# Kernel tuning notes

Measured on AMD Instinct MI355X. Metric: run time of the kernel, lower is better.

The kernel has to match this reference:

```python
import jax, jax.numpy as jnp
import numpy as np

D = 256  # subgraph_width
N_CLASSES = 10
EPS = 1e-5  # torch LayerNorm default


def _layernorm(x, g, b):
    mu = jnp.mean(x, axis=-1, keepdims=True)
    var = jnp.var(x, axis=-1, keepdims=True)
    return (x - mu) * jax.lax.rsqrt(var + EPS) * g + b


def setup_inputs() -> dict:
    key = jax.random.key(0)
    ks = jax.random.split(key, 16)
    B, T, N = 64, 512, 512
    traj = jax.random.normal(ks[0], (B, T, 2), dtype=jnp.float32)
    labels = jax.random.randint(ks[1], (B,), 0, N_CLASSES)
    h = jax.random.normal(ks[2], (B, N, D), dtype=jnp.float32)
    valid_len = jnp.maximum(jax.random.randint(ks[3], (B,), 0, N), 1)
    s = 0.02
    params = dict(
        emb=jax.random.normal(ks[4], (N_CLASSES, D), dtype=jnp.float32) * s,
        w_mlp=jax.random.normal(ks[5], (2, D), dtype=jnp.float32) * s,
        b_mlp=jnp.zeros((D,), jnp.float32),
        ln_g=jnp.ones((D,), jnp.float32),
        ln_b=jnp.zeros((D,), jnp.float32),
        wq=jax.random.normal(ks[6], (D, D), dtype=jnp.float32) * s,
        bq=jnp.zeros((D,), jnp.float32),
        wk=jax.random.normal(ks[7], (D, D), dtype=jnp.float32) * s,
        bk=jnp.zeros((D,), jnp.float32),
        wv=jax.random.normal(ks[8], (D, D), dtype=jnp.float32) * s,
        bv=jnp.zeros((D,), jnp.float32),
        w_out=jax.random.normal(ks[9], (D, 1), dtype=jnp.float32) * s,
        b_out=jnp.zeros((1,), jnp.float32),
    )
    return dict(traj=traj, labels=labels, h=h, valid_len=valid_len, **params)


def reference(traj, labels, h, valid_len, emb, w_mlp, b_mlp, ln_g, ln_b,
              wq, bq, wk, bk, wv, bv, w_out, b_out):
    # MLP(in=2, out=D, activation='leaky'): Linear -> LayerNorm -> LeakyReLU
    x = jax.nn.leaky_relu(_layernorm(traj @ w_mlp + b_mlp, ln_g, ln_b))  # [B,T,D]
    le = emb[labels]                          # [B,D]
    x = x + le[:, None, :]                    # embed-add
    # SelfAttentionWithKeyFCLayer: Q from x, K/V from h, scaled, key-masked by valid_len
    q = x @ wq + bq                            # [B,T,D]
    k = h @ wk + bk                            # [B,N,D]
    v = h @ wv + bv                            # [B,N,D]
    scores = jnp.einsum('btd,bnd->btn', q, k) / jnp.sqrt(jnp.float32(D))
    N = h.shape[1]
    key_mask = jnp.arange(N)[None, :] < valid_len[:, None]          # [B,N]
    scores = jnp.where(key_mask[:, None, :], scores, jnp.float32(-1e9))
    attn = jax.nn.softmax(scores, axis=-1)
    enc = jnp.einsum('btn,bnd->btd', attn, v)  # [B,T,D]
    pooled = jnp.max(enc, axis=1) + le          # [B,D]
    return jax.nn.sigmoid(pooled @ w_out + b_out)  # [B,1]
```

## Files before the change

kernel.cpp:

```cpp
#include <hip/hip_runtime.h>
#include <math.h>

typedef float f32x4 __attribute__((ext_vector_type(4)));
typedef __bf16 bf16x8 __attribute__((ext_vector_type(8)));
typedef unsigned short u16x8 __attribute__((ext_vector_type(8)));
typedef unsigned short u16x4 __attribute__((ext_vector_type(4)));
typedef unsigned int u32x4 __attribute__((ext_vector_type(4)));

#define MFMA(a, b, c) __builtin_amdgcn_mfma_f32_16x16x32_bf16((a), (b), (c), 0, 0, 0)

static __device__ __forceinline__ unsigned short f2bf(float f) {
  unsigned u = __float_as_uint(f);
  u += 0x7FFFu + ((u >> 16) & 1u);
  return (unsigned short)(u >> 16);
}
static __device__ __forceinline__ float bf2f(unsigned short s) {
  return __uint_as_float(((unsigned)s) << 16);
}
static __device__ __forceinline__ unsigned pack2bf(float lo, float hi) {
  return (unsigned)f2bf(lo) | ((unsigned)f2bf(hi) << 16);
}

static __device__ __forceinline__ int swz512(int row, int col) {
  return row * 512 + (col ^ ((((row & 7) ^ (col >> 6)) & 7) << 4));
}
static __device__ __forceinline__ int swzV(int d, int col) {
  return d * 64 + (col ^ (((d >> 1) & 3) << 4));
}
static __device__ __forceinline__ int swzO(int d, int col) {
  return d * 256 + (col ^ ((((d & 7) ^ (col >> 7)) & 7) << 4));
}

__global__ __launch_bounds__(256) void setup(
    const float* __restrict__ w0m, const float* __restrict__ w1m, const float* __restrict__ w2m,
    unsigned short* __restrict__ t0m, unsigned short* __restrict__ t1m, unsigned short* __restrict__ t2m,
    const float* __restrict__ w_mlp, const float* __restrict__ b_mlp, float* __restrict__ lnsc,
    const int* __restrict__ vlen, int* __restrict__ tasktab) {
  int bid = blockIdx.x;
  int t = threadIdx.x;
  if (bid == 48) {
    float w0 = w_mlp[t], w1 = w_mlp[256 + t], bb = b_mlp[t];
    float v[9] = {w0, w1, bb, w0 * w0, w1 * w1, w0 * w1, w0 * bb, w1 * bb, bb * bb};
    __shared__ float red[4][9];
#pragma unroll
    for (int j = 0; j < 9; ++j) {
      float s = v[j];
#pragma unroll
      for (int off = 32; off >= 1; off >>= 1) s += __shfl_xor(s, off, 64);
      v[j] = s;
    }
    if ((t & 63) == 0)
      for (int j = 0; j < 9; ++j) red[t >> 6][j] = v[j];
    __syncthreads();
    if (t < 9) lnsc[t] = red[0][t] + red[1][t] + red[2][t] + red[3][t];
    return;
  }
  if (bid == 49) {
    __shared__ int srank[64];
    if (t < 64) {
      int vb = vlen[t], r = 0;
      for (int j = 0; j < 64; ++j) {
        int vj = vlen[j];
        r += (vj > vb) || (vj == vb && j < t);
      }
      srank[r] = t;
    }
    __syncthreads();
    if (t < 64) {
      int r = t, b = srank[r];
      int xcd = r & 7, a = r >> 3;
      for (int tt = 0; tt < 4; ++tt)
        tasktab[(a * 4 + tt) * 8 + xcd] = (b << 2) | tt;
    }
    return;
  }
  int m = bid >> 4, t16 = bid & 15;
  const float* w = (m == 0) ? w0m : (m == 1) ? w1m : w2m;
  unsigned short* o = (m == 0) ? t0m : (m == 1) ? t1m : t2m;
  __shared__ float sm[64][65];
  int bi = t16 >> 2, bj = t16 & 3;
  for (int kb = 0; kb < 16; ++kb) {
    int idx = kb * 256 + t;
    int r = idx >> 6, c = idx & 63;
    sm[r][c] = w[(bi * 64 + r) * 256 + bj * 64 + c];
  }
  __syncthreads();
  for (int kb = 0; kb < 16; ++kb) {
    int idx = kb * 256 + t;
    int r = idx >> 6, c = idx & 63;
    int d = bj * 64 + r, e = bi * 64 + c;
    o[(e >> 5) * 8192 + d * 32 + (e & 31)] = f2bf(sm[c][r]);
  }
}

static __device__ __forceinline__ void gemm_direct(
    const unsigned short* __restrict__ Bpk, const unsigned short* Alds,
    int w, int g, int c15, f32x4 (&acc)[4][4]) {
  const unsigned short* bp = Bpk + (w * 64 + c15) * 32 + 8 * g;
#pragma unroll
  for (int c = 0; c < 8; ++c) {
    bf16x8 bfv[4];
#pragma unroll
    for (int nt = 0; nt < 4; ++nt)
      bfv[nt] = *(const bf16x8*)(bp + c * 8192 + nt * 512);
    bf16x8 af[4];
#pragma unroll
    for (int at = 0; at < 4; ++at)
      af[at] = *(const bf16x8*)((char*)Alds + swz512(at * 16 + c15, c * 64 + 16 * g));
    __builtin_amdgcn_s_setprio(1);
#pragma unroll
    for (int at = 0; at < 4; ++at)
#pragma unroll
      for (int nt = 0; nt < 4; ++nt) acc[at][nt] = MFMA(af[at], bfv[nt], acc[at][nt]);
    __builtin_amdgcn_s_setprio(0);
  }
}

__global__ __launch_bounds__(512, 4) void gemms(
    const float* __restrict__ h, const int* __restrict__ vlen,
    const unsigned short* __restrict__ wkPk, const float* __restrict__ bk,
    const unsigned short* __restrict__ wvPk, const float* __restrict__ bv,
    unsigned short* __restrict__ kout, unsigned short* __restrict__ vT) {
  __shared__ unsigned short Alds[64 * 256];
  __shared__ unsigned short Klds[64 * 256];
  int tid = threadIdx.x, w = tid >> 6, lane = tid & 63, g = lane >> 4, c15 = lane & 15;
  int tile = blockIdx.x;
  int b = tile >> 3;
  int nbase = (tile & 7) * 64;
  if (nbase >= vlen[b]) return;
  f32x4 acc[4][4];
  {
    const float* hb = h + (size_t)tile * 16384;
    f32x4 ha[4], hc[4];
#pragma unroll
    for (int i = 0; i < 4; ++i) {
      ha[i] = *(const f32x4*)(hb + i * 4096 + tid * 8);
      hc[i] = *(const f32x4*)(hb + i * 4096 + tid * 8 + 4);
    }
#pragma unroll
    for (int i = 0; i < 4; ++i) {
      u16x8 pk;
#pragma unroll
      for (int j = 0; j < 4; ++j) { pk[j] = f2bf(ha[i][j]); pk[j + 4] = f2bf(hc[i][j]); }
      *(u16x8*)((char*)Alds + swz512(i * 16 + (tid >> 5), (tid & 31) * 16)) = pk;
    }
  }
#pragma unroll
  for (int a = 0; a < 4; ++a)
#pragma unroll
    for (int n = 0; n < 4; ++n) acc[a][n] = (f32x4){0.f, 0.f, 0.f, 0.f};
  __syncthreads();

  int w4 = w & 3;
  if (w < 4) {
    gemm_direct(wvPk, Alds, w4, g, c15, acc);
#pragma unroll
    for (int at = 0; at < 4; ++at)
#pragma unroll
      for (int nt = 0; nt < 4; ++nt) {
        int col = w4 * 64 + nt * 16 + c15;
        float bb = bv[col];
        u16x4 o;
#pragma unroll
        for (int r = 0; r < 4; ++r) o[r] = f2bf(acc[at][nt][r] + bb);
        *(u16x4*)(vT + (size_t)b * 131072 + (size_t)col * 512 + nbase + at * 16 + 4 * g) = o;
      }
  } else {
    gemm_direct(wkPk, Alds, w4, g, c15, acc);
#pragma unroll
    for (int at = 0; at < 4; ++at)
#pragma unroll
      for (int nt = 0; nt < 4; ++nt) {
        int col = w4 * 64 + nt * 16 + c15;
        float bb = bk[col];
#pragma unroll
        for (int r = 0; r < 4; ++r)
          *(unsigned short*)((char*)Klds + swz512(at * 16 + 4 * g + r, col * 2)) =
              f2bf(acc[at][nt][r] + bb);
      }
  }
  __syncthreads();
  if (tid < 256) {
    int row = tid >> 2;
    for (int i = 0; i < 8; ++i) {
      int colb = (tid & 3) * 128 + i * 16;
      u16x8 vv = *(const u16x8*)((char*)Klds + swz512(row, colb));
      *(u16x8*)(kout + (size_t)(tile * 64 + row) * 256 + colb / 2) = vv;
    }
  }
}

__global__ __launch_bounds__(512, 2) void attn(
    const float* __restrict__ traj, const int* __restrict__ labels,
    const float* __restrict__ emb, const float* __restrict__ w_mlp,
    const float* __restrict__ b_mlp, const float* __restrict__ ln_g,
    const float* __restrict__ ln_b, const float* __restrict__ lnsc,
    const unsigned short* __restrict__ wqPk, const float* __restrict__ bq,
    const unsigned short* __restrict__ k, const unsigned short* __restrict__ vT,
    const int* __restrict__ valid_len, const int* __restrict__ tasktab,
    float* __restrict__ partial) {
  __shared__ unsigned short buf[2][16384];

  int task = tasktab[blockIdx.x];
  int b = task >> 2, tt = task & 3;
  int tid = threadIdx.x, w = tid >> 6, lane = tid & 63, g = lane >> 4, c15 = lane & 15;
  int vl = valid_len[b];
  int nit = (vl + 31) >> 5;
  int wq4 = w & 3;

  {
    int rrow = tid >> 5, cb = (tid & 31) * 8;
    int lab = labels[b];
    f32x4 wa0 = *(const f32x4*)(w_mlp + cb), wa1 = *(const f32x4*)(w_mlp + cb + 4);
    f32x4 wb0 = *(const f32x4*)(w_mlp + 256 + cb), wb1 = *(const f32x4*)(w_mlp + 256 + cb + 4);
    f32x4 bm0 = *(const f32x4*)(b_mlp + cb), bm1 = *(const f32x4*)(b_mlp + cb + 4);
    f32x4 g0 = *(const f32x4*)(ln_g + cb), g1 = *(const f32x4*)(ln_g + cb + 4);
    f32x4 lb0 = *(const f32x4*)(ln_b + cb), lb1 = *(const f32x4*)(ln_b + cb + 4);
    f32x4 le0 = *(const f32x4*)(emb + lab * 256 + cb), le1 = *(const f32x4*)(emb + lab * 256 + cb + 4);
    float s0 = lnsc[0], s1 = lnsc[1], s2 = lnsc[2], s3 = lnsc[3], s4_ = lnsc[4],
          s5 = lnsc[5], s6 = lnsc[6], s7 = lnsc[7], s8 = lnsc[8];
#pragma unroll
    for (int i = 0; i < 8; ++i) {
      int row = i * 16 + rrow, grow = b * 512 + tt * 128 + row;
      float t0 = traj[grow * 2], t1 = traj[grow * 2 + 1];
      float mu = (t0 * s0 + t1 * s1 + s2) * (1.f / 256.f);
      float ea2 = (t0 * t0 * s3 + t1 * t1 * s4_ + s8 +
                   2.f * (t0 * t1 * s5 + t0 * s6 + t1 * s7)) * (1.f / 256.f);
      float rstd = rsqrtf(ea2 - mu * mu + 1e-5f);
      u16x8 pk;
#pragma unroll
      for (int j = 0; j < 4; ++j) {
        float a0 = t0 * wa0[j] + t1 * wb0[j] + bm0[j];
        float y0 = (a0 - mu) * rstd * g0[j] + lb0[j];
        pk[j] = f2bf((y0 > 0.f ? y0 : 0.01f * y0) + le0[j]);
        float a1 = t0 * wa1[j] + t1 * wb1[j] + bm1[j];
        float y1 = (a1 - mu) * rstd * g1[j] + lb1[j];
        pk[j + 4] = f2bf((y1 > 0.f ? y1 : 0.01f * y1) + le1[j]);
      }
      *(u16x8*)((char*)buf + swz512(row, cb * 2)) = pk;
    }
  }
  __syncthreads();

  {
    f32x4 qacc[4][4];
#pragma unroll
    for (int a = 0; a < 4; ++a)
#pragma unroll
      for (int n = 0; n < 4; ++n) qacc[a][n] = (f32x4){0.f, 0.f, 0.f, 0.f};
    int rbase = (w >> 2) * 64;
    const unsigned short* bp = wqPk + (wq4 * 64 + c15) * 32 + 8 * g;
#pragma unroll
    for (int c = 0; c < 8; ++c) {
      bf16x8 bfv[4];
#pragma unroll
      for (int nt = 0; nt < 4; ++nt)
        bfv[nt] = *(const bf16x8*)(bp + c * 8192 + nt * 512);
      bf16x8 af[4];
#pragma unroll
      for (int at = 0; at < 4; ++at)
        af[at] = *(const bf16x8*)((char*)buf + swz512(rbase + at * 16 + c15, c * 64 + 16 * g));
      __builtin_amdgcn_s_setprio(1);
#pragma unroll
      for (int at = 0; at < 4; ++at)
#pragma unroll
        for (int nt = 0; nt < 4; ++nt) qacc[at][nt] = MFMA(af[at], bfv[nt], qacc[at][nt]);
      __builtin_amdgcn_s_setprio(0);
    }
    __syncthreads();
#pragma unroll
    for (int nt = 0; nt < 4; ++nt) {
      int col = wq4 * 64 + nt * 16 + c15;
      float bb = bq[col];
#pragma unroll
      for (int at = 0; at < 4; ++at)
#pragma unroll
        for (int r = 0; r < 4; ++r)
          *(unsigned short*)((char*)buf + swz512(rbase + at * 16 + 4 * g + r, col * 2)) =
              f2bf(qacc[at][nt][r] + bb);
    }
  }
  __syncthreads();
  bf16x8 qf[8];
#pragma unroll
  for (int kk = 0; kk < 8; ++kk)
    qf[kk] = *(const bf16x8*)((char*)buf + swz512(w * 16 + c15, kk * 64 + 16 * g));
  __syncthreads();

  f32x4 acco[16];
#pragma unroll
  for (int i = 0; i < 16; ++i) acco[i] = (f32x4){0.f, 0.f, 0.f, 0.f};
  float rs = 0.f;

  const unsigned short* kbase = k + (size_t)b * 512 * 256;
  const unsigned short* vbase = vT + (size_t)b * 131072;
  u16x8 kpre[2], vpre[2];

#pragma unroll
  for (int i = 0; i < 2; ++i) {
    int idx = tid + 512 * i, key = idx >> 5, s = idx & 31;
    kpre[i] = *(const u16x8*)(kbase + (size_t)key * 256 + s * 8);
  }
#pragma unroll
  for (int i = 0; i < 2; ++i) {
    int idx = tid + 512 * i, d = idx >> 2, s = idx & 3;
    vpre[i] = *(const u16x8*)(vbase + (size_t)d * 512 + s * 8);
  }
#pragma unroll
  for (int i = 0; i < 2; ++i) {
    int idx = tid + 512 * i, key = idx >> 5, s = idx & 31;
    *(u16x8*)((char*)buf[0] + swz512(key, s * 16)) = kpre[i];
  }
#pragma unroll
  for (int i = 0; i < 2; ++i) {
    int idx = tid + 512 * i, d = idx >> 2, s = idx & 3;
    *(u16x8*)((char*)(buf[0] + 8192) + swzV(d, s * 16)) = vpre[i];
  }

  for (int it = 0; it < nit; ++it) {
    int cur = it & 1;
    __syncthreads();
    bool pf = (it + 1 < nit);
    if (pf) {
      int n1 = (it + 1) * 32;
#pragma unroll
      for (int i = 0; i < 2; ++i) {
        int idx = tid + 512 * i, key = idx >> 5, s = idx & 31;
        kpre[i] = *(const u16x8*)(kbase + (size_t)(n1 + key) * 256 + s * 8);
      }
#pragma unroll
      for (int i = 0; i < 2; ++i) {
        int idx = tid + 512 * i, d = idx >> 2, s = idx & 3;
        vpre[i] = *(const u16x8*)(vbase + (size_t)d * 512 + n1 + s * 8);
      }
    }
    unsigned short* Klds = buf[cur];
    unsigned short* Vlds = buf[cur] + 8192;
    int n0 = it * 32;

    float p[2][4];
    unsigned u01[2], u23[2];
#pragma unroll
    for (int c = 0; c < 2; ++c) {
      f32x4 s4 = (f32x4){0.f, 0.f, 0.f, 0.f};
      __builtin_amdgcn_s_setprio(1);
#pragma unroll
      for (int kk = 0; kk < 8; ++kk) {
        bf16x8 kf = *(const bf16x8*)((char*)Klds + swz512(c * 16 + c15, kk * 64 + 16 * g));
        s4 = MFMA(kf, qf[kk], s4);
      }
      __builtin_amdgcn_s_setprio(0);
#pragma unroll
      for (int r = 0; r < 4; ++r) {
        int key = n0 + c * 16 + 4 * g + r;
        float pv = (key < vl) ? __expf(s4[r] * 0.0625f) : 0.f;
        p[c][r] = pv;
        rs += pv;
      }
      u01[c] = pack2bf(p[c][0], p[c][1]);
      u23[c] = pack2bf(p[c][2], p[c][3]);
    }
    int srcA = c15 | ((lane & 16) << 1);
    int srcB = srcA + 16;
    unsigned x0a = (unsigned)__shfl((int)u01[0], srcA, 64);
    unsigned x1a = (unsigned)__shfl((int)u01[1], srcA, 64);
    unsigned x0b = (unsigned)__shfl((int)u23[0], srcA, 64);
    unsigned x1b = (unsigned)__shfl((int)u23[1], srcA, 64);
    unsigned x0c = (unsigned)__shfl((int)u01[0], srcB, 64);
    unsigned x1c = (unsigned)__shfl((int)u01[1], srcB, 64);
    unsigned x0d = (unsigned)__shfl((int)u23[0], srcB, 64);
    unsigned x1d = (unsigned)__shfl((int)u23[1], srcB, 64);
    bool hi = g >= 2;
    union { u32x4 u; bf16x8 v; } pa;
    pa.u[0] = hi ? x1a : x0a;
    pa.u[1] = hi ? x1b : x0b;
    pa.u[2] = hi ? x1c : x0c;
    pa.u[3] = hi ? x1d : x0d;
    __builtin_amdgcn_s_setprio(1);
#pragma unroll
    for (int dt = 0; dt < 16; ++dt) {
      bf16x8 vf = *(const bf16x8*)((char*)Vlds + swzV(dt * 16 + c15, 16 * g));
      acco[dt] = MFMA(vf, pa.v, acco[dt]);
    }
    __builtin_amdgcn_s_setprio(0);
    if (pf) {
      unsigned short* Kn = buf[cur ^ 1];
      unsigned short* Vn = buf[cur ^ 1] + 8192;
#pragma unroll
      for (int i = 0; i < 2; ++i) {
        int idx = tid + 512 * i, key = idx >> 5, s = idx & 31;
        *(u16x8*)((char*)Kn + swz512(key, s * 16)) = kpre[i];
      }
#pragma unroll
      for (int i = 0; i < 2; ++i) {
        int idx = tid + 512 * i, d = idx >> 2, s = idx & 3;
        *(u16x8*)((char*)Vn + swzV(d, s * 16)) = vpre[i];
      }
    }
  }
  rs += __shfl_xor(rs, 16, 64);
  rs += __shfl_xor(rs, 32, 64);
  float inv = 1.f / rs;
  __syncthreads();
  int qcol = w * 16 + c15;
#pragma unroll
  for (int dt = 0; dt < 16; ++dt)
#pragma unroll
    for (int r = 0; r < 4; ++r) {
      int d = dt * 16 + 4 * g + r;
      *(unsigned short*)((char*)buf + swzO(d, qcol * 2)) = f2bf(acco[dt][r] * inv);
    }
  __syncthreads();
  {
    int d = tid & 255, half = tid >> 8;
    float m = -1e30f;
    for (int i = 0; i < 8; ++i) {
      u16x8 vv = *(const u16x8*)((char*)buf + swzO(d, half * 128 + i * 16));
#pragma unroll
      for (int j = 0; j < 8; ++j) m = fmaxf(m, bf2f(vv[j]));
    }
    partial[(((size_t)b * 4 + tt) * 2 + half) * 256 + d] = m;
  }
}

__global__ __launch_bounds__(256) void finalize(
    const float* __restrict__ partial, const float* __restrict__ emb,
    const int* __restrict__ labels, const float* __restrict__ w_out,
    const float* __restrict__ b_out, float* __restrict__ out) {
  int b = blockIdx.x, t = threadIdx.x;
  float m = -1e30f;
#pragma unroll
  for (int s8 = 0; s8 < 8; ++s8)
    m = fmaxf(m, partial[((size_t)b * 8 + s8) * 256 + t]);
  m += emb[labels[b] * 256 + t];
  __shared__ float red[256];
  red[t] = m * w_out[t];
  __syncthreads();
  for (int s = 128; s > 0; s >>= 1) {
    if (t < s) red[t] += red[t + s];
    __syncthreads();
  }
  if (t == 0) out[b] = 1.f / (1.f + __expf(-(red[0] + b_out[0])));
}

extern "C" void kernel_launch(void* const* d_in, const int* in_sizes, int n_in,
                              void* d_out, int out_size, void* d_ws, size_t ws_size,
                              hipStream_t stream) {
  const float* traj   = (const float*)d_in[0];
  const int*   labels = (const int*)d_in[1];
  const float* h      = (const float*)d_in[2];
  const int*   vlen   = (const int*)d_in[3];
  const float* emb    = (const float*)d_in[4];
  const float* w_mlp  = (const float*)d_in[5];
  const float* b_mlp  = (const float*)d_in[6];
  const float* ln_g   = (const float*)d_in[7];
  const float* ln_b   = (const float*)d_in[8];
  const float* wq     = (const float*)d_in[9];
  const float* bq     = (const float*)d_in[10];
  const float* wk     = (const float*)d_in[11];
  const float* bk     = (const float*)d_in[12];
  const float* wv     = (const float*)d_in[13];
  const float* bv     = (const float*)d_in[14];
  const float* w_out  = (const float*)d_in[15];
  const float* b_out  = (const float*)d_in[16];
  float* out = (float*)d_out;

  unsigned short* kb   = (unsigned short*)d_ws;
  unsigned short* vT   = kb + (size_t)32768 * 256;
  unsigned short* wqPk = vT + (size_t)32768 * 256;
  unsigned short* wkPk = wqPk + 65536;
  unsigned short* wvPk = wkPk + 65536;
  float* lnsc    = (float*)(wvPk + 65536);
  float* partial = lnsc + 16;
  int*   tasktab = (int*)(partial + 64 * 8 * 256);

  setup<<<50, 256, 0, stream>>>(wq, wk, wv, wqPk, wkPk, wvPk, w_mlp, b_mlp, lnsc,
                                vlen, tasktab);
  gemms<<<512, 512, 0, stream>>>(h, vlen, wkPk, bk, wvPk, bv, kb, vT);
  attn<<<256, 512, 0, stream>>>(traj, labels, emb, w_mlp, b_mlp, ln_g, ln_b, lnsc,
                                wqPk, bq, kb, vT, vlen, tasktab, partial);
  finalize<<<64, 256, 0, stream>>>(partial, emb, labels, w_out, b_out, out);
}
```

Measured before the change: 72.88 us.

## Software-pipeline attention loop with triple LDS buffer and packed bf16 convert

Restructures the key loop into a three-slot LDS ring so the QK^T MFMAs and softmax for the next tile are issued alongside the PV MFMAs of the current tile. Global prefetch now runs two tiles ahead and there is one barrier per iteration. It also swaps the software bf16 rounding for the hardware v_cvt_pk_bf16_f32 instruction. LDS per block rises from 64KB to 96KB, which may limit the two-blocks-per-CU occupancy requested by the launch bounds.

```diff
diff --git a/kernel.cpp b/kernel.cpp
--- a/kernel.cpp
+++ b/kernel.cpp
@@ -17,8 +17,10 @@
 static __device__ __forceinline__ float bf2f(unsigned short s) {
   return __uint_as_float(((unsigned)s) << 16);
 }
-static __device__ __forceinline__ unsigned pack2bf(float lo, float hi) {
-  return (unsigned)f2bf(lo) | ((unsigned)f2bf(hi) << 16);
+static __device__ __forceinline__ unsigned cvt_pk(float lo, float hi) {
+  unsigned r;
+  asm("v_cvt_pk_bf16_f32 %0, %1, %2" : "=v"(r) : "v"(lo), "v"(hi));
+  return r;
 }
 
 static __device__ __forceinline__ int swz512(int row, int col) {
@@ -199,7 +201,7 @@
     const unsigned short* __restrict__ k, const unsigned short* __restrict__ vT,
     const int* __restrict__ valid_len, const int* __restrict__ tasktab,
     float* __restrict__ partial) {
-  __shared__ unsigned short buf[2][16384];
+  __shared__ unsigned short buf[3][16384];
 
   int task = tasktab[blockIdx.x];
   int b = task >> 2, tt = task & 3;
@@ -295,70 +297,62 @@
   const unsigned short* kbase = k + (size_t)b * 512 * 256;
   const unsigned short* vbase = vT + (size_t)b * 131072;
   u16x8 kpre[2], vpre[2];
-
-#pragma unroll
-  for (int i = 0; i < 2; ++i) {
-    int idx = tid + 512 * i, key = idx >> 5, s = idx & 31;
-    kpre[i] = *(const u16x8*)(kbase + (size_t)key * 256 + s * 8);
-  }
-#pragma unroll
-  for (int i = 0; i < 2; ++i) {
-    int idx = tid + 512 * i, d = idx >> 2, s = idx & 3;
-    vpre[i] = *(const u16x8*)(vbase + (size_t)d * 512 + s * 8);
-  }
-#pragma unroll
-  for (int i = 0; i < 2; ++i) {
-    int idx = tid + 512 * i, key = idx >> 5, s = idx & 31;
-    *(u16x8*)((char*)buf[0] + swz512(key, s * 16)) = kpre[i];
-  }
-#pragma unroll
-  for (int i = 0; i < 2; ++i) {
-    int idx = tid + 512 * i, d = idx >> 2, s = idx & 3;
-    *(u16x8*)((char*)(buf[0] + 8192) + swzV(d, s * 16)) = vpre[i];
-  }
-
-  for (int it = 0; it < nit; ++it) {
-    int cur = it & 1;
-    __syncthreads();
-    bool pf = (it + 1 < nit);
-    if (pf) {
-      int n1 = (it + 1) * 32;
-#pragma unroll
-      for (int i = 0; i < 2; ++i) {
-        int idx = tid + 512 * i, key = idx >> 5, s = idx & 31;
-        kpre[i] = *(const u16x8*)(kbase + (size_t)(n1 + key) * 256 + s * 8);
-      }
-#pragma unroll
-      for (int i = 0; i < 2; ++i) {
-        int idx = tid + 512 * i, d = idx >> 2, s = idx & 3;
-        vpre[i] = *(const u16x8*)(vbase + (size_t)d * 512 + n1 + s * 8);
-      }
-    }
-    unsigned short* Klds = buf[cur];
-    unsigned short* Vlds = buf[cur] + 8192;
-    int n0 = it * 32;
-
-    float p[2][4];
+  f32x4 s4[2];
+  union Pa { u32x4 u; bf16x8 v; } paC;
+
+  auto STAGE_REGS = [&](int n0) {
+#pragma unroll
+    for (int i = 0; i < 2; ++i) {
+      int idx = tid + 512 * i, key = idx >> 5, s = idx & 31;
+      kpre[i] = *(const u16x8*)(kbase + (size_t)(n0 + key) * 256 + s * 8);
+    }
+#pragma unroll
+    for (int i = 0; i < 2; ++i) {
+      int idx = tid + 512 * i, d = idx >> 2, s = idx & 3;
+      vpre[i] = *(const u16x8*)(vbase + (size_t)d * 512 + n0 + s * 8);
+    }
+  };
+  auto WRITE = [&](int slot) {
+    char* base = (char*)buf + slot * 32768;
+#pragma unroll
+    for (int i = 0; i < 2; ++i) {
+      int idx = tid + 512 * i, key = idx >> 5, s = idx & 31;
+      *(u16x8*)(base + swz512(key, s * 16)) = kpre[i];
+    }
+#pragma unroll
+    for (int i = 0; i < 2; ++i) {
+      int idx = tid + 512 * i, d = idx >> 2, s = idx & 3;
+      *(u16x8*)(base + 16384 + swzV(d, s * 16)) = vpre[i];
+    }
+  };
+  auto QKT = [&](int slot) {
+    const char* base = (const char*)buf + slot * 32768;
+    s4[0] = (f32x4){0.f, 0.f, 0.f, 0.f};
+    s4[1] = (f32x4){0.f, 0.f, 0.f, 0.f};
+    __builtin_amdgcn_s_setprio(1);
+#pragma unroll
+    for (int c = 0; c < 2; ++c)
+#pragma unroll
+      for (int kk = 0; kk < 8; ++kk) {
+        bf16x8 kf = *(const bf16x8*)(base + swz512(c * 16 + c15, kk * 64 + 16 * g));
+        s4[c] = MFMA(kf, qf[kk], s4[c]);
+      }
+    __builtin_amdgcn_s_setprio(0);
+  };
+  auto SOFTMAX = [&](int n0) {
     unsigned u01[2], u23[2];
 #pragma unroll
     for (int c = 0; c < 2; ++c) {
-      f32x4 s4 = (f32x4){0.f, 0.f, 0.f, 0.f};
-      __builtin_amdgcn_s_setprio(1);
-#pragma unroll
-      for (int kk = 0; kk < 8; ++kk) {
-        bf16x8 kf = *(const bf16x8*)((char*)Klds + swz512(c * 16 + c15, kk * 64 + 16 * g));
-        s4 = MFMA(kf, qf[kk], s4);
-      }
-      __builtin_amdgcn_s_setprio(0);
+      float p4[4];
 #pragma unroll
       for (int r = 0; r < 4; ++r) {
         int key = n0 + c * 16 + 4 * g + r;
-        float pv = (key < vl) ? __expf(s4[r] * 0.0625f) : 0.f;
-        p[c][r] = pv;
+        float pv = (key < vl) ? __expf(s4[c][r] * 0.0625f) : 0.f;
+        p4[r] = pv;
         rs += pv;
       }
-      u01[c] = pack2bf(p[c][0], p[c][1]);
-      u23[c] = pack2bf(p[c][2], p[c][3]);
+      u01[c] = cvt_pk(p4[0], p4[1]);
+      u23[c] = cvt_pk(p4[2], p4[3]);
     }
     int srcA = c15 | ((lane & 16) << 1);
     int srcB = srcA + 16;
@@ -371,33 +365,38 @@
     unsigned x0d = (unsigned)__shfl((int)u23[0], srcB, 64);
     unsigned x1d = (unsigned)__shfl((int)u23[1], srcB, 64);
     bool hi = g >= 2;
-    union { u32x4 u; bf16x8 v; } pa;
-    pa.u[0] = hi ? x1a : x0a;
-    pa.u[1] = hi ? x1b : x0b;
-    pa.u[2] = hi ? x1c : x0c;
-    pa.u[3] = hi ? x1d : x0d;
+    paC.u[0] = hi ? x1a : x0a;
+    paC.u[1] = hi ? x1b : x0b;
+    paC.u[2] = hi ? x1c : x0c;
+    paC.u[3] = hi ? x1d : x0d;
+  };
+  auto PV = [&](int slot) {
+    const char* base = (const char*)buf + slot * 32768 + 16384;
     __builtin_amdgcn_s_setprio(1);
 #pragma unroll
     for (int dt = 0; dt < 16; ++dt) {
-      bf16x8 vf = *(const bf16x8*)((char*)Vlds + swzV(dt * 16 + c15, 16 * g));
-      acco[dt] = MFMA(vf, pa.v, acco[dt]);
+      bf16x8 vf = *(const bf16x8*)(base + swzV(dt * 16 + c15, 16 * g));
+      acco[dt] = MFMA(vf, paC.v, acco[dt]);
     }
     __builtin_amdgcn_s_setprio(0);
-    if (pf) {
-      unsigned short* Kn = buf[cur ^ 1];
-      unsigned short* Vn = buf[cur ^ 1] + 8192;
-#pragma unroll
-      for (int i = 0; i < 2; ++i) {
-        int idx = tid + 512 * i, key = idx >> 5, s = idx & 31;
-        *(u16x8*)((char*)Kn + swz512(key, s * 16)) = kpre[i];
-      }
-#pragma unroll
-      for (int i = 0; i < 2; ++i) {
-        int idx = tid + 512 * i, d = idx >> 2, s = idx & 3;
-        *(u16x8*)((char*)Vn + swzV(d, s * 16)) = vpre[i];
-      }
-    }
-  }
+  };
+
+  STAGE_REGS(0);
+  WRITE(0);
+  if (nit > 1) STAGE_REGS(32);
+  __syncthreads();
+  QKT(0);
+  SOFTMAX(0);
+
+  for (int it = 0; it < nit; ++it) {
+    if (it + 1 < nit) WRITE((it + 1) % 3);
+    if (it + 2 < nit) STAGE_REGS((it + 2) * 32);
+    __syncthreads();
+    if (it + 1 < nit) QKT((it + 1) % 3);
+    PV(it % 3);
+    if (it + 1 < nit) SOFTMAX((it + 1) * 32);
+  }
+
   rs += __shfl_xor(rs, 16, 64);
   rs += __shfl_xor(rs, 32, 64);
   float inv = 1.f / rs;
```

Measured after the change: 71.66 us. Within noise of the previous version (-1.7%).

## Split attention into 512 blocks of 64 queries with balanced task pairing

Applied to the files above, without the earlier changes.

The attention kernel moves from 256 blocks of 512 threads (128 queries each) to 512 blocks of 256 threads (64 queries each). Per-thread K/V prefetch doubles to cover the 32-key tile, and the task table pairs long and short batches so work spreads more evenly. It also swaps the software bf16 pack for the v_cvt_pk_bf16_f32 instruction and shrinks the output-transpose swizzle. Each key tile is now loaded by more blocks, which adds memory traffic, and each thread holds more prefetch registers.

```diff
diff --git a/kernel.cpp b/kernel.cpp
--- a/kernel.cpp
+++ b/kernel.cpp
@@ -17,8 +17,10 @@
 static __device__ __forceinline__ float bf2f(unsigned short s) {
   return __uint_as_float(((unsigned)s) << 16);
 }
-static __device__ __forceinline__ unsigned pack2bf(float lo, float hi) {
-  return (unsigned)f2bf(lo) | ((unsigned)f2bf(hi) << 16);
+static __device__ __forceinline__ unsigned cvt_pk(float lo, float hi) {
+  unsigned r;
+  asm("v_cvt_pk_bf16_f32 %0, %1, %2" : "=v"(r) : "v"(lo), "v"(hi));
+  return r;
 }
 
 static __device__ __forceinline__ int swz512(int row, int col) {
@@ -27,8 +29,8 @@
 static __device__ __forceinline__ int swzV(int d, int col) {
   return d * 64 + (col ^ (((d >> 1) & 3) << 4));
 }
-static __device__ __forceinline__ int swzO(int d, int col) {
-  return d * 256 + (col ^ ((((d & 7) ^ (col >> 7)) & 7) << 4));
+static __device__ __forceinline__ int swzO64(int d, int col) {
+  return d * 128 + (col ^ ((d & 7) << 4));
 }
 
 __global__ __launch_bounds__(256) void setup(
@@ -67,10 +69,14 @@
     }
     __syncthreads();
     if (t < 64) {
-      int r = t, b = srank[r];
+      int r = t;
+      int b1 = srank[r];
+      int b2 = srank[63 - r];
       int xcd = r & 7, a = r >> 3;
-      for (int tt = 0; tt < 4; ++tt)
-        tasktab[(a * 4 + tt) * 8 + xcd] = (b << 2) | tt;
+      for (int tt = 0; tt < 4; ++tt) {
+        tasktab[(a * 4 + tt) * 8 + xcd] = (b1 << 3) | tt;
+        tasktab[256 + (a * 4 + tt) * 8 + xcd] = (b2 << 3) | (tt + 4);
+      }
     }
     return;
   }
@@ -190,7 +196,7 @@
   }
 }
 
-__global__ __launch_bounds__(512, 2) void attn(
+__global__ __launch_bounds__(256, 2) void attn(
     const float* __restrict__ traj, const int* __restrict__ labels,
     const float* __restrict__ emb, const float* __restrict__ w_mlp,
     const float* __restrict__ b_mlp, const float* __restrict__ ln_g,
@@ -202,11 +208,10 @@
   __shared__ unsigned short buf[2][16384];
 
   int task = tasktab[blockIdx.x];
-  int b = task >> 2, tt = task & 3;
+  int b = task >> 3, tt = task & 7;
   int tid = threadIdx.x, w = tid >> 6, lane = tid & 63, g = lane >> 4, c15 = lane & 15;
   int vl = valid_len[b];
   int nit = (vl + 31) >> 5;
-  int wq4 = w & 3;
 
   {
     int rrow = tid >> 5, cb = (tid & 31) * 8;
@@ -221,7 +226,7 @@
           s5 = lnsc[5], s6 = lnsc[6], s7 = lnsc[7], s8 = lnsc[8];
 #pragma unroll
     for (int i = 0; i < 8; ++i) {
-      int row = i * 16 + rrow, grow = b * 512 + tt * 128 + row;
+      int row = i * 8 + rrow, grow = b * 512 + tt * 64 + row;
       float t0 = traj[grow * 2], t1 = traj[grow * 2 + 1];
       float mu = (t0 * s0 + t1 * s1 + s2) * (1.f / 256.f);
       float ea2 = (t0 * t0 * s3 + t1 * t1 * s4_ + s8 +
@@ -248,35 +253,17 @@
     for (int a = 0; a < 4; ++a)
 #pragma unroll
       for (int n = 0; n < 4; ++n) qacc[a][n] = (f32x4){0.f, 0.f, 0.f, 0.f};
-    int rbase = (w >> 2) * 64;
-    const unsigned short* bp = wqPk + (wq4 * 64 + c15) * 32 + 8 * g;
-#pragma unroll
-    for (int c = 0; c < 8; ++c) {
-      bf16x8 bfv[4];
-#pragma unroll
-      for (int nt = 0; nt < 4; ++nt)
-        bfv[nt] = *(const bf16x8*)(bp + c * 8192 + nt * 512);
-      bf16x8 af[4];
+    gemm_direct(wqPk, (const unsigned short*)buf, w, g, c15, qacc);
+    __syncthreads();
+#pragma unroll
+    for (int nt = 0; nt < 4; ++nt) {
+      int col = w * 64 + nt * 16 + c15;
+      float bb = bq[col];
 #pragma unroll
       for (int at = 0; at < 4; ++at)
-        af[at] = *(const bf16x8*)((char*)buf + swz512(rbase + at * 16 + c15, c * 64 + 16 * g));
-      __builtin_amdgcn_s_setprio(1);
-#pragma unroll
-      for (int at = 0; at < 4; ++at)
-#pragma unroll
-        for (int nt = 0; nt < 4; ++nt) qacc[at][nt] = MFMA(af[at], bfv[nt], qacc[at][nt]);
-      __builtin_amdgcn_s_setprio(0);
-    }
-    __syncthreads();
-#pragma unroll
-    for (int nt = 0; nt < 4; ++nt) {
-      int col = wq4 * 64 + nt * 16 + c15;
-      float bb = bq[col];
-#pragma unroll
-      for (int at = 0; at < 4; ++at)
 #pragma unroll
         for (int r = 0; r < 4; ++r)
-          *(unsigned short*)((char*)buf + swz512(rbase + at * 16 + 4 * g + r, col * 2)) =
+          *(unsigned short*)((char*)buf + 32768 + swz512(at * 16 + 4 * g + r, col * 2)) =
               f2bf(qacc[at][nt][r] + bb);
     }
   }
@@ -284,7 +271,7 @@
   bf16x8 qf[8];
 #pragma unroll
   for (int kk = 0; kk < 8; ++kk)
-    qf[kk] = *(const bf16x8*)((char*)buf + swz512(w * 16 + c15, kk * 64 + 16 * g));
+    qf[kk] = *(const bf16x8*)((char*)buf + 32768 + swz512(w * 16 + c15, kk * 64 + 16 * g));
   __syncthreads();
 
   f32x4 acco[16];
@@ -294,26 +281,26 @@
 
   const unsigned short* kbase = k + (size_t)b * 512 * 256;
   const unsigned short* vbase = vT + (size_t)b * 131072;
-  u16x8 kpre[2], vpre[2];
-
-#pragma unroll
-  for (int i = 0; i < 2; ++i) {
-    int idx = tid + 512 * i, key = idx >> 5, s = idx & 31;
+  u16x8 kpre[4], vpre[4];
+
+#pragma unroll
+  for (int i = 0; i < 4; ++i) {
+    int idx = tid + 256 * i, key = idx >> 5, s = idx & 31;
     kpre[i] = *(const u16x8*)(kbase + (size_t)key * 256 + s * 8);
   }
 #pragma unroll
-  for (int i = 0; i < 2; ++i) {
-    int idx = tid + 512 * i, d = idx >> 2, s = idx & 3;
+  for (int i = 0; i < 4; ++i) {
+    int idx = tid + 256 * i, d = idx >> 2, s = idx & 3;
     vpre[i] = *(const u16x8*)(vbase + (size_t)d * 512 + s * 8);
   }
 #pragma unroll
-  for (int i = 0; i < 2; ++i) {
-    int idx = tid + 512 * i, key = idx >> 5, s = idx & 31;
+  for (int i = 0; i < 4; ++i) {
+    int idx = tid + 256 * i, key = idx >> 5, s = idx & 31;
     *(u16x8*)((char*)buf[0] + swz512(key, s * 16)) = kpre[i];
   }
 #pragma unroll
-  for (int i = 0; i < 2; ++i) {
-    int idx = tid + 512 * i, d = idx >> 2, s = idx & 3;
+  for (int i = 0; i < 4; ++i) {
+    int idx = tid + 256 * i, d = idx >> 2, s = idx & 3;
     *(u16x8*)((char*)(buf[0] + 8192) + swzV(d, s * 16)) = vpre[i];
   }
 
@@ -324,13 +311,13 @@
     if (pf) {
       int n1 = (it + 1) * 32;
 #pragma unroll
-      for (int i = 0; i < 2; ++i) {
-        int idx = tid + 512 * i, key = idx >> 5, s = idx & 31;
+      for (int i = 0; i < 4; ++i) {
+        int idx = tid + 256 * i, key = idx >> 5, s = idx & 31;
         kpre[i] = *(const u16x8*)(kbase + (size_t)(n1 + key) * 256 + s * 8);
       }
 #pragma unroll
-      for (int i = 0; i < 2; ++i) {
-        int idx = tid + 512 * i, d = idx >> 2, s = idx & 3;
+      for (int i = 0; i < 4; ++i) {
+        int idx = tid + 256 * i, d = idx >> 2, s = idx & 3;
         vpre[i] = *(const u16x8*)(vbase + (size_t)d * 512 + n1 + s * 8);
       }
     }
@@ -357,8 +344,8 @@
         p[c][r] = pv;
         rs += pv;
       }
-      u01[c] = pack2bf(p[c][0], p[c][1]);
-      u23[c] = pack2bf(p[c][2], p[c][3]);
+      u01[c] = cvt_pk(p[c][0], p[c][1]);
+      u23[c] = cvt_pk(p[c][2], p[c][3]);
     }
     int srcA = c15 | ((lane & 16) << 1);
     int srcB = srcA + 16;
@@ -387,13 +374,13 @@
       unsigned short* Kn = buf[cur ^ 1];
       unsigned short* Vn = buf[cur ^ 1] + 8192;
 #pragma unroll
-      for (int i = 0; i < 2; ++i) {
-        int idx = tid + 512 * i, key = idx >> 5, s = idx & 31;
+      for (int i = 0; i < 4; ++i) {
+        int idx = tid + 256 * i, key = idx >> 5, s = idx & 31;
         *(u16x8*)((char*)Kn + swz512(key, s * 16)) = kpre[i];
       }
 #pragma unroll
-      for (int i = 0; i < 2; ++i) {
-        int idx = tid + 512 * i, d = idx >> 2, s = idx & 3;
+      for (int i = 0; i < 4; ++i) {
+        int idx = tid + 256 * i, d = idx >> 2, s = idx & 3;
         *(u16x8*)((char*)Vn + swzV(d, s * 16)) = vpre[i];
       }
     }
@@ -408,18 +395,18 @@
 #pragma unroll
     for (int r = 0; r < 4; ++r) {
       int d = dt * 16 + 4 * g + r;
-      *(unsigned short*)((char*)buf + swzO(d, qcol * 2)) = f2bf(acco[dt][r] * inv);
+      *(unsigned short*)((char*)buf + swzO64(d, qcol * 2)) = f2bf(acco[dt][r] * inv);
     }
   __syncthreads();
   {
-    int d = tid & 255, half = tid >> 8;
+    int d = tid;
     float m = -1e30f;
     for (int i = 0; i < 8; ++i) {
-      u16x8 vv = *(const u16x8*)((char*)buf + swzO(d, half * 128 + i * 16));
+      u16x8 vv = *(const u16x8*)((char*)buf + swzO64(d, i * 16));
 #pragma unroll
       for (int j = 0; j < 8; ++j) m = fmaxf(m, bf2f(vv[j]));
     }
-    partial[(((size_t)b * 4 + tt) * 2 + half) * 256 + d] = m;
+    partial[((size_t)b * 8 + tt) * 256 + d] = m;
   }
 }
 
@@ -477,7 +464,7 @@
   setup<<<50, 256, 0, stream>>>(wq, wk, wv, wqPk, wkPk, wvPk, w_mlp, b_mlp, lnsc,
                                 vlen, tasktab);
   gemms<<<512, 512, 0, stream>>>(h, vlen, wkPk, bk, wvPk, bv, kb, vT);
-  attn<<<256, 512, 0, stream>>>(traj, labels, emb, w_mlp, b_mlp, ln_g, ln_b, lnsc,
+  attn<<<512, 256, 0, stream>>>(traj, labels, emb, w_mlp, b_mlp, ln_g, ln_b, lnsc,
                                 wqPk, bq, kb, vT, vlen, tasktab, partial);
   finalize<<<64, 256, 0, stream>>>(partial, emb, labels, w_out, b_out, out);
 }
```

After: 68.81 us. -5.6%, faster.
